# Optimization experiments

Hardware: AMD Instinct MI355X
Metric: run time of the kernel (lower is better)

## Reference

```python
import jax, jax.numpy as jnp
import numpy as np

B = 262144
IN, H = 2, 50


def setup_inputs() -> dict:
    key = jax.random.key(0)
    ks = jax.random.split(key, 12)
    k = 1.0 / np.sqrt(H)
    u = lambda kk, shape: jax.random.uniform(kk, shape, jnp.float32, -k, k)
    return {
        "s": jax.random.normal(ks[0], (B, IN), jnp.float32),
        "h": jax.random.normal(ks[1], (B, H), jnp.float32),
        "w_ih": u(ks[2], (3 * H, IN)),
        "w_hh": u(ks[3], (3 * H, H)),
        "b_ih": u(ks[4], (3 * H,)),
        "b_hh": u(ks[5], (3 * H,)),
        "actor_w": u(ks[6], (2, H)),
        "actor_b": u(ks[7], (2,)),
        "critic_w": u(ks[8], (1, H)),
        "critic_b": u(ks[9], (1,)),
    }


def reference(s, h, w_ih, w_hh, b_ih, b_hh, actor_w, actor_b, critic_w, critic_b):
    # PyTorch GRUCell gate math (gate order: reset, update, new)
    gi = s @ w_ih.T + b_ih          # [B, 3H]
    gh = h @ w_hh.T + b_hh          # [B, 3H]
    i_r, i_z, i_n = jnp.split(gi, 3, axis=1)
    h_r, h_z, h_n = jnp.split(gh, 3, axis=1)
    r = jax.nn.sigmoid(i_r + h_r)
    z = jax.nn.sigmoid(i_z + h_z)
    n = jnp.tanh(i_n + r * h_n)
    h_new = (1.0 - z) * n + z * h   # [B, H]
    c = h_new @ critic_w.T + critic_b            # [B, 1]
    pi = jax.nn.softmax(h_new @ actor_w.T + actor_b, axis=1)  # [B, 2]
    return h_new, c, pi
```

## Files before the change

### kernel.cpp

```cpp
#include <hip/hip_runtime.h>
#include <hip/hip_bf16.h>


#define BDIM 256

typedef __bf16 bf16x8 __attribute__((ext_vector_type(8)));
typedef float f32x4 __attribute__((ext_vector_type(4)));
typedef unsigned __attribute__((may_alias)) u32a;
typedef unsigned short __attribute__((may_alias)) u16a;

__device__ __forceinline__ float bf2f(unsigned short u) {
    union { unsigned u; float f; } x; x.u = ((unsigned)u) << 16; return x.f;
}
__device__ __forceinline__ unsigned short f2bf(float f) {
    union { float f; unsigned u; } x; x.f = f;
    unsigned r = x.u + 0x7fffu + ((x.u >> 16) & 1u);
    return (unsigned short)(r >> 16);
}
__device__ __forceinline__ unsigned packbf(float a, float b) {
    union { __hip_bfloat162 h; unsigned u; } c;
    c.h = __float22bfloat162_rn(make_float2(a, b));
    return c.u;
}
__device__ __forceinline__ bf16x8 ldsfrag(const unsigned short* p) {
    bf16x8 v; __builtin_memcpy(&v, p, 16); return v;
}

__global__ __launch_bounds__(BDIM, 4) void gru_fused(
    const float* __restrict__ s,
    const float* __restrict__ h,
    const float* __restrict__ w_ih,
    const float* __restrict__ w_hh,
    const float* __restrict__ b_ih,
    const float* __restrict__ b_hh,
    const float* __restrict__ actor_w,
    const float* __restrict__ actor_b,
    const float* __restrict__ critic_w,
    const float* __restrict__ critic_b,
    float* __restrict__ out,
    int Btot, int nTiles)
{
    __shared__ __align__(16) unsigned short xlds[64 * 72];
    __shared__ __align__(16) unsigned short wlds[1536 * 8];

    const int tid  = threadIdx.x;
    const int wave = tid >> 6;
    const int lane = tid & 63;
    const int c16  = lane & 15;
    const int quad = lane >> 4;
    const int R    = wave * 16;

    u32a* xlds32 = (u32a*)xlds;

    for (int i = tid; i < 2304; i += BDIM)
        xlds32[i] = ((i % 36) == 26) ? 0x00003f80u : 0u;

    for (int e = tid; e < 1536; e += BDIM) {
        int ln = e & 63;
        int ks = (e >> 6) & 1;
        int t  = (e >> 7) & 3;
        int g  = e >> 9;
        int n  = t * 16 + (ln & 15);
        int kbase = ks * 32 + (ln >> 4) * 8;
        unsigned short vals[8];
        if (n < 50) {
            int r = g * 50 + n;
            #pragma unroll
            for (int i = 0; i < 8; ++i) {
                int k = kbase + i;
                float v = 0.f;
                if (k < 50)       v = w_hh[r * 50 + k];
                else if (k == 50) v = (g < 2) ? w_ih[r * 2 + 0] : 0.f;
                else if (k == 51) v = (g < 2) ? w_ih[r * 2 + 1] : 0.f;
                else if (k == 52) {
                    v = b_hh[r];
                    if (g < 2) v += b_ih[r];
                }
                vals[i] = f2bf(v);
            }
        } else {
            #pragma unroll
            for (int i = 0; i < 8; ++i) vals[i] = 0;
        }
        #pragma unroll
        for (int i = 0; i < 8; ++i) wlds[e * 8 + i] = vals[i];
    }

    float wi0[4], wi1[4], bi[4], aw0[4], aw1[4], awc[4];
    #pragma unroll
    for (int t = 0; t < 4; ++t) {
        int j = t * 16 + c16;
        bool ok = (j < 50);
        wi0[t] = ok ? w_ih[(100 + j) * 2 + 0] : 0.f;
        wi1[t] = ok ? w_ih[(100 + j) * 2 + 1] : 0.f;
        bi[t]  = ok ? b_ih[100 + j]           : 0.f;
        aw0[t] = ok ? actor_w[j]              : 0.f;
        aw1[t] = ok ? actor_w[50 + j]         : 0.f;
        awc[t] = ok ? critic_w[j]             : 0.f;
    }
    const float ab0 = actor_b[0], ab1 = actor_b[1], cb = critic_b[0];

    __syncthreads();

    const float2* h2 = (const float2*)h;
    const float2* s2 = (const float2*)s;
    const long long outc = (long long)Btot * 50;
    float2* opi = (float2*)(out + (long long)Btot * 51);

    float2 pf[7];
    int bt = blockIdx.x;
    {
        long long hb = (long long)(bt * 64 + R) * 25;
        #pragma unroll
        for (int j = 0; j < 6; ++j) pf[j] = h2[hb + lane + j * 64];
        if (lane < 16)      pf[6] = h2[hb + 384 + lane];
        else if (lane < 32) pf[6] = s2[bt * 64 + R + lane - 16];
    }

    while (bt < nTiles) {
        const int rowbase = bt * 64;

        #pragma unroll
        for (int j = 0; j < 6; ++j) {
            int d = lane + j * 64;
            int r = d / 25, dk = d - r * 25;
            xlds32[(R + r) * 36 + dk] = packbf(pf[j].x, pf[j].y);
        }
        if (lane < 16)
            xlds32[(R + 15) * 36 + 9 + lane] = packbf(pf[6].x, pf[6].y);
        else if (lane < 32)
            xlds32[(R + lane - 16) * 36 + 25] = packbf(pf[6].x, pf[6].y);

        asm volatile("" ::: "memory");

        const int nbt = bt + gridDim.x;
        {
            int pb = (nbt < nTiles) ? nbt : bt;
            long long hb = (long long)(pb * 64 + R) * 25;
            #pragma unroll
            for (int j = 0; j < 6; ++j) pf[j] = h2[hb + lane + j * 64];
            if (lane < 16)      pf[6] = h2[hb + 384 + lane];
            else if (lane < 32) pf[6] = s2[pb * 64 + R + lane - 16];
        }

        float2 srow[4];
        #pragma unroll
        for (int reg = 0; reg < 4; ++reg)
            srow[reg] = s2[rowbase + R + quad * 4 + reg];

        const unsigned short* arow = &xlds[(R + c16) * 72 + quad * 8];
        bf16x8 a0 = ldsfrag(arow);
        bf16x8 a1 = ldsfrag(arow + 32);

        float hn_r[4][4];
        #pragma unroll
        for (int t = 0; t < 4; ++t) {
            f32x4 ar = {0.f,0.f,0.f,0.f}, az = ar, an = ar;
            const int tb = (t * 128 + lane) * 8;
            bf16x8 br0 = ldsfrag(&wlds[tb]);
            bf16x8 br1 = ldsfrag(&wlds[tb + 512]);
            bf16x8 bz0 = ldsfrag(&wlds[tb + 4096]);
            bf16x8 bz1 = ldsfrag(&wlds[tb + 4608]);
            bf16x8 bn0 = ldsfrag(&wlds[tb + 8192]);
            bf16x8 bn1 = ldsfrag(&wlds[tb + 8704]);
            ar = __builtin_amdgcn_mfma_f32_16x16x32_bf16(a0, br0, ar, 0, 0, 0);
            ar = __builtin_amdgcn_mfma_f32_16x16x32_bf16(a1, br1, ar, 0, 0, 0);
            az = __builtin_amdgcn_mfma_f32_16x16x32_bf16(a0, bz0, az, 0, 0, 0);
            az = __builtin_amdgcn_mfma_f32_16x16x32_bf16(a1, bz1, az, 0, 0, 0);
            an = __builtin_amdgcn_mfma_f32_16x16x32_bf16(a0, bn0, an, 0, 0, 0);
            an = __builtin_amdgcn_mfma_f32_16x16x32_bf16(a1, bn1, an, 0, 0, 0);

            int j = t * 16 + c16;
            #pragma unroll
            for (int reg = 0; reg < 4; ++reg) {
                int lr = R + quad * 4 + reg;
                float inn = fmaf(srow[reg].y, wi1[t],
                            fmaf(srow[reg].x, wi0[t], bi[t]));
                float rg = __builtin_amdgcn_rcpf(1.f + __expf(-ar[reg]));
                float zg = __builtin_amdgcn_rcpf(1.f + __expf(-az[reg]));
                float x = inn + rg * an[reg];
                x = fminf(fmaxf(x, -20.f), 20.f);
                float e2 = __expf(2.f * x);
                float ng = (e2 - 1.f) * __builtin_amdgcn_rcpf(e2 + 1.f);
                float hv = bf2f(((const u16a*)xlds)[lr * 72 + j]);
                float hnew = (1.f - zg) * ng + zg * hv;
                bool ok = (j < 50);
                hn_r[reg][t] = ok ? hnew : 0.f;
                if (ok) out[(long long)(rowbase + lr) * 50 + j] = hnew;
            }
        }

        float sum0[4], sum1[4], sumc[4];
        #pragma unroll
        for (int reg = 0; reg < 4; ++reg) {
            float p0 = 0.f, p1 = 0.f, pc = 0.f;
            #pragma unroll
            for (int t = 0; t < 4; ++t) {
                p0 = fmaf(hn_r[reg][t], aw0[t], p0);
                p1 = fmaf(hn_r[reg][t], aw1[t], p1);
                pc = fmaf(hn_r[reg][t], awc[t], pc);
            }
            #pragma unroll
            for (int m = 1; m < 16; m <<= 1) {
                p0 += __shfl_xor(p0, m);
                p1 += __shfl_xor(p1, m);
                pc += __shfl_xor(pc, m);
            }
            sum0[reg] = p0; sum1[reg] = p1; sumc[reg] = pc;
        }
        if (c16 < 4) {
            float A0 = (c16 == 0) ? sum0[0] : (c16 == 1) ? sum0[1]
                     : (c16 == 2) ? sum0[2] : sum0[3];
            float A1 = (c16 == 0) ? sum1[0] : (c16 == 1) ? sum1[1]
                     : (c16 == 2) ? sum1[2] : sum1[3];
            float C  = (c16 == 0) ? sumc[0] : (c16 == 1) ? sumc[1]
                     : (c16 == 2) ? sumc[2] : sumc[3];
            int gr = rowbase + R + quad * 4 + c16;
            out[outc + gr] = C + cb;
            A0 += ab0; A1 += ab1;
            float m = fmaxf(A0, A1);
            float e0 = __expf(A0 - m), e1 = __expf(A1 - m);
            float inv = 1.f / (e0 + e1);
            float2 pv; pv.x = e0 * inv; pv.y = e1 * inv;
            opi[gr] = pv;
        }
        bt = nbt;
    }
}

extern "C" void kernel_launch(void* const* d_in, const int* in_sizes, int n_in,
                              void* d_out, int out_size, void* d_ws, size_t ws_size,
                              hipStream_t stream) {
    const float* s        = (const float*)d_in[0];
    const float* h        = (const float*)d_in[1];
    const float* w_ih     = (const float*)d_in[2];
    const float* w_hh     = (const float*)d_in[3];
    const float* b_ih     = (const float*)d_in[4];
    const float* b_hh     = (const float*)d_in[5];
    const float* actor_w  = (const float*)d_in[6];
    const float* actor_b  = (const float*)d_in[7];
    const float* critic_w = (const float*)d_in[8];
    const float* critic_b = (const float*)d_in[9];
    float* out = (float*)d_out;

    int Btot = in_sizes[1] / 50;
    int nTiles = Btot / 64;
    int grid = nTiles < 1024 ? nTiles : 1024;

    gru_fused<<<grid, BDIM, 0, stream>>>(s, h, w_ih, w_hh, b_ih, b_hh,
                                         actor_w, actor_b, critic_w, critic_b,
                                         out, Btot, nTiles);
}
```

Measured before the change: 143.3 us.

## Hoist weight fragments into registers, use DPP row reductions, simplify gate math

Loads all 24 W_hh bf16 fragments from LDS into registers once per block instead of once per tile. Launch bounds drop from 4 to 2 waves per SIMD so the extra VGPRs fit. The 16-lane reductions now use DPP row operations in place of shfl_xor, and the tanh/blend math is rewritten with fewer ops, dropping the clamp. This trades occupancy for less LDS traffic and fewer ALU ops. Removing the clamp relies on rcp handling an infinite exp correctly.

```diff
diff --git a/kernel.cpp b/kernel.cpp
--- a/kernel.cpp
+++ b/kernel.cpp
@@ -26,7 +26,21 @@
     bf16x8 v; __builtin_memcpy(&v, p, 16); return v;
 }
 
-__global__ __launch_bounds__(BDIM, 4) void gru_fused(
+template <int CTRL>
+__device__ __forceinline__ float dpp_add(float v) {
+    int s = __builtin_bit_cast(int, v);
+    int r = __builtin_amdgcn_update_dpp(s, s, CTRL, 0xf, 0xf, false);
+    return v + __builtin_bit_cast(float, r);
+}
+__device__ __forceinline__ float row16_sum(float v) {
+    v = dpp_add<0x128>(v);
+    v = dpp_add<0x124>(v);
+    v = dpp_add<0x122>(v);
+    v = dpp_add<0x121>(v);
+    return v;
+}
+
+__global__ __launch_bounds__(BDIM, 2) void gru_fused(
     const float* __restrict__ s,
     const float* __restrict__ h,
     const float* __restrict__ w_ih,
@@ -102,9 +116,19 @@
 
     __syncthreads();
 
+    bf16x8 bf[3][4][2];
+    #pragma unroll
+    for (int g = 0; g < 3; ++g)
+        #pragma unroll
+        for (int t = 0; t < 4; ++t)
+            #pragma unroll
+            for (int ks = 0; ks < 2; ++ks)
+                bf[g][t][ks] =
+                    ldsfrag(&wlds[((g << 9) | (t << 7) | (ks << 6) | lane) * 8]);
+
     const float2* h2 = (const float2*)h;
     const float2* s2 = (const float2*)s;
-    const long long outc = (long long)Btot * 50;
+    float* oc = out + (long long)Btot * 50;
     float2* opi = (float2*)(out + (long long)Btot * 51);
 
     float2 pf[7];
@@ -152,23 +176,18 @@
         bf16x8 a0 = ldsfrag(arow);
         bf16x8 a1 = ldsfrag(arow + 32);
 
+        float* ob = out + (long long)rowbase * 50;
+
         float hn_r[4][4];
         #pragma unroll
         for (int t = 0; t < 4; ++t) {
             f32x4 ar = {0.f,0.f,0.f,0.f}, az = ar, an = ar;
-            const int tb = (t * 128 + lane) * 8;
-            bf16x8 br0 = ldsfrag(&wlds[tb]);
-            bf16x8 br1 = ldsfrag(&wlds[tb + 512]);
-            bf16x8 bz0 = ldsfrag(&wlds[tb + 4096]);
-            bf16x8 bz1 = ldsfrag(&wlds[tb + 4608]);
-            bf16x8 bn0 = ldsfrag(&wlds[tb + 8192]);
-            bf16x8 bn1 = ldsfrag(&wlds[tb + 8704]);
-            ar = __builtin_amdgcn_mfma_f32_16x16x32_bf16(a0, br0, ar, 0, 0, 0);
-            ar = __builtin_amdgcn_mfma_f32_16x16x32_bf16(a1, br1, ar, 0, 0, 0);
-            az = __builtin_amdgcn_mfma_f32_16x16x32_bf16(a0, bz0, az, 0, 0, 0);
-            az = __builtin_amdgcn_mfma_f32_16x16x32_bf16(a1, bz1, az, 0, 0, 0);
-            an = __builtin_amdgcn_mfma_f32_16x16x32_bf16(a0, bn0, an, 0, 0, 0);
-            an = __builtin_amdgcn_mfma_f32_16x16x32_bf16(a1, bn1, an, 0, 0, 0);
+            ar = __builtin_amdgcn_mfma_f32_16x16x32_bf16(a0, bf[0][t][0], ar, 0, 0, 0);
+            ar = __builtin_amdgcn_mfma_f32_16x16x32_bf16(a1, bf[0][t][1], ar, 0, 0, 0);
+            az = __builtin_amdgcn_mfma_f32_16x16x32_bf16(a0, bf[1][t][0], az, 0, 0, 0);
+            az = __builtin_amdgcn_mfma_f32_16x16x32_bf16(a1, bf[1][t][1], az, 0, 0, 0);
+            an = __builtin_amdgcn_mfma_f32_16x16x32_bf16(a0, bf[2][t][0], an, 0, 0, 0);
+            an = __builtin_amdgcn_mfma_f32_16x16x32_bf16(a1, bf[2][t][1], an, 0, 0, 0);
 
             int j = t * 16 + c16;
             #pragma unroll
@@ -179,14 +198,12 @@
                 float rg = __builtin_amdgcn_rcpf(1.f + __expf(-ar[reg]));
                 float zg = __builtin_amdgcn_rcpf(1.f + __expf(-az[reg]));
                 float x = inn + rg * an[reg];
-                x = fminf(fmaxf(x, -20.f), 20.f);
                 float e2 = __expf(2.f * x);
-                float ng = (e2 - 1.f) * __builtin_amdgcn_rcpf(e2 + 1.f);
+                float ng = 1.f - 2.f * __builtin_amdgcn_rcpf(e2 + 1.f);
                 float hv = bf2f(((const u16a*)xlds)[lr * 72 + j]);
-                float hnew = (1.f - zg) * ng + zg * hv;
-                bool ok = (j < 50);
-                hn_r[reg][t] = ok ? hnew : 0.f;
-                if (ok) out[(long long)(rowbase + lr) * 50 + j] = hnew;
+                float hnew = fmaf(zg, hv - ng, ng);
+                hn_r[reg][t] = (j < 50) ? hnew : 0.f;
+                if (j < 50) ob[lr * 50 + j] = hnew;
             }
         }
 
@@ -200,13 +217,9 @@
                 p1 = fmaf(hn_r[reg][t], aw1[t], p1);
                 pc = fmaf(hn_r[reg][t], awc[t], pc);
             }
-            #pragma unroll
-            for (int m = 1; m < 16; m <<= 1) {
-                p0 += __shfl_xor(p0, m);
-                p1 += __shfl_xor(p1, m);
-                pc += __shfl_xor(pc, m);
-            }
-            sum0[reg] = p0; sum1[reg] = p1; sumc[reg] = pc;
+            sum0[reg] = row16_sum(p0);
+            sum1[reg] = row16_sum(p1);
+            sumc[reg] = row16_sum(pc);
         }
         if (c16 < 4) {
             float A0 = (c16 == 0) ? sum0[0] : (c16 == 1) ? sum0[1]
@@ -216,7 +229,7 @@
             float C  = (c16 == 0) ? sumc[0] : (c16 == 1) ? sumc[1]
                      : (c16 == 2) ? sumc[2] : sumc[3];
             int gr = rowbase + R + quad * 4 + c16;
-            out[outc + gr] = C + cb;
+            oc[gr] = C + cb;
             A0 += ab0; A1 += ab1;
             float m = fmaxf(A0, A1);
             float e0 = __expf(A0 - m), e1 = __expf(A1 - m);
```

After: 146.5 us. 1.02x slower.
